# Kernel tuning notes

Hardware: AMD Instinct MI355X
Metric: run time of the kernel (lower is better)

## Reference

```python
import jax, jax.numpy as jnp
import numpy as np
from jax import lax

T = 256        # sentence length
V = 50000      # vocab
NT = 50        # POS tags
NL = 40        # dependency labels
WD, TD = 300, 100
IN = WD + TD   # 400, LSTM input & hidden size
H = IN
BI = 2 * H     # 800, biLSTM output per token
MI = 2 * BI    # 1600, MLP input/hidden size


def setup_inputs() -> dict:
    key = jax.random.key(0)
    ks = jax.random.split(key, 32)
    s = 0.05
    d = {
        'words': jax.random.randint(ks[0], (T,), 0, V),
        'tags': jax.random.randint(ks[1], (T,), 0, NT),
        'arcs': jax.random.randint(ks[2], (T + 1,), 0, T + 1),
        'h0': jax.random.normal(ks[3], (4, 1, H), jnp.float32),
        'c0': jax.random.normal(ks[4], (4, 1, H), jnp.float32),
        'word_emb': jax.random.normal(ks[5], (V, WD), jnp.float32) * s,
        'tag_emb': jax.random.normal(ks[6], (NT, TD), jnp.float32) * s,
        # LSTM layer 0: input IN; layer 1: input BI. Leading dim 2 = directions (fwd, rev).
        'Wih0': jax.random.normal(ks[7], (2, 4 * H, IN), jnp.float32) * s,
        'Whh0': jax.random.normal(ks[8], (2, 4 * H, H), jnp.float32) * s,
        'bih0': jax.random.normal(ks[9], (2, 4 * H), jnp.float32) * s,
        'bhh0': jax.random.normal(ks[10], (2, 4 * H), jnp.float32) * s,
        'Wih1': jax.random.normal(ks[11], (2, 4 * H, BI), jnp.float32) * s,
        'Whh1': jax.random.normal(ks[12], (2, 4 * H, H), jnp.float32) * s,
        'bih1': jax.random.normal(ks[13], (2, 4 * H), jnp.float32) * s,
        'bhh1': jax.random.normal(ks[14], (2, 4 * H), jnp.float32) * s,
        # arc-score MLP: 1600 -> 1600 -> 1 (Linear, Tanh, Linear)
        'Wa1': jax.random.normal(ks[15], (MI, MI), jnp.float32) * s,
        'ba1': jax.random.normal(ks[16], (MI,), jnp.float32) * s,
        'Wa2': jax.random.normal(ks[17], (1, MI), jnp.float32) * s,
        'ba2': jax.random.normal(ks[18], (1,), jnp.float32) * s,
        # label MLP: 1600 -> 1600 -> 40
        'Wl1': jax.random.normal(ks[19], (MI, MI), jnp.float32) * s,
        'bl1': jax.random.normal(ks[20], (MI,), jnp.float32) * s,
        'Wl2': jax.random.normal(ks[21], (NL, MI), jnp.float32) * s,
        'bl2': jax.random.normal(ks[22], (NL,), jnp.float32) * s,
    }
    return d


def _lstm_dir(x, Wih, Whh, bih, bhh, h, c):
    # x: [T, in]; returns [T, H]. Torch gate order i, f, g, o.
    xg = x @ Wih.T + (bih + bhh)  # precompute input projection: [T, 4H]

    def step(carry, xt):
        h, c = carry
        g = xt + h @ Whh.T
        i, f, gg, o = jnp.split(g, 4, axis=-1)
        i, f, o = jax.nn.sigmoid(i), jax.nn.sigmoid(f), jax.nn.sigmoid(o)
        c = f * c + i * jnp.tanh(gg)
        h = o * jnp.tanh(c)
        return (h, c), h

    (_, _), ys = lax.scan(step, (h, c), xg)
    return ys


def _bilstm_layer(x, Wih, Whh, bih, bhh, h0f, c0f, h0b, c0b):
    fwd = _lstm_dir(x, Wih[0], Whh[0], bih[0], bhh[0], h0f, c0f)
    bwd = _lstm_dir(x[::-1], Wih[1], Whh[1], bih[1], bhh[1], h0b, c0b)[::-1]
    return jnp.concatenate([fwd, bwd], axis=-1)


def _mlp(z, W1, b1, W2, b2):
    return jnp.tanh(z @ W1.T + b1) @ W2.T + b2


def reference(words, tags, arcs, h0, c0, word_emb, tag_emb,
              Wih0, Whh0, bih0, bhh0, Wih1, Whh1, bih1, bhh1,
              Wa1, ba1, Wa2, ba2, Wl1, bl1, Wl2, bl2):
    n = words.shape[0]
    x = jnp.concatenate([word_emb[words], tag_emb[tags]], axis=-1)  # [T, 400]
    x1 = _bilstm_layer(x, Wih0, Whh0, bih0, bhh0, h0[0, 0], c0[0, 0], h0[1, 0], c0[1, 0])
    hV = _bilstm_layer(x1, Wih1, Whh1, bih1, bhh1, h0[2, 0], c0[2, 0], h0[3, 0], c0[3, 0])  # [T, 800]

    # All-pairs arc scores: feats[h, d] = concat(hV[h], hV[d]) -> MLP -> scalar.
    hh = jnp.broadcast_to(hV[:, None, :], (n, n, BI))
    dd = jnp.broadcast_to(hV[None, :, :], (n, n, BI))
    feats = jnp.concatenate([hh, dd], axis=-1)  # [T, T, 1600]
    raw = _mlp(feats, Wa1, ba1, Wa2, ba2)[..., 0]  # [T, T]
    raw = raw * (1.0 - jnp.eye(n, dtype=raw.dtype))  # head == dep left at 0
    scores = jnp.zeros((n + 1, n + 1), raw.dtype).at[1:, 1:].set(raw).at[0, 0].set(1.0)

    # Labels: for token i with gold head h (1-based), concat(hV[i], hV[h-1]); head==0 -> zeros.
    heads = arcs[1:]
    idx = jnp.clip(heads - 1, 0, n - 1)
    lf = jnp.concatenate([hV, hV[idx]], axis=-1)  # [T, 1600]
    lab = _mlp(lf, Wl1, bl1, Wl2, bl2)  # [T, 40]
    lab = jnp.where((heads == 0)[:, None], jnp.zeros_like(lab), lab)
    return (scores, lab)
```

## Files before the change

### kernel.cpp

```cpp
#include <hip/hip_runtime.h>

typedef unsigned int   u32;
typedef unsigned long long u64;

__device__ __forceinline__ float fast_tanh(float x) {
    x = fminf(fmaxf(x, -15.f), 15.f);
    float e = __expf(2.f * x);
    return __fdividef(e - 1.f, e + 1.f);
}

#define OF_X    ((size_t)0)
#define OF_XG   (OF_X  + 409600)
#define OF_H    (OF_XG + 3276800)
#define OF_P    (OF_H  + 1638400)
#define OF_Q    (OF_P  + 1638400)
#define OF_U    (OF_Q  + 1638400)

__device__ __forceinline__ float4 hist4(const u64* __restrict__ hist, int t, int k) {
    const u64* p = (k < 400) ? hist + (size_t)t * 400 + k
                             : hist + 102400 + (size_t)(255 - t) * 400 + (k - 400);
    ulonglong2 a = *(const ulonglong2*)p;
    ulonglong2 b = *(const ulonglong2*)(p + 2);
    return make_float4(__uint_as_float((u32)a.x), __uint_as_float((u32)a.y),
                       __uint_as_float((u32)b.x), __uint_as_float((u32)b.y));
}

__global__ void embed_kernel(const int* __restrict__ words, const int* __restrict__ tags,
                             const float* __restrict__ wemb, const float* __restrict__ temb,
                             float* __restrict__ x) {
    int t = blockIdx.x;
    int w = words[t], tg = tags[t];
    for (int i = threadIdx.x; i < 400; i += 256) {
        float v = (i < 300) ? wemb[(size_t)w * 300 + i]
                            : temb[(size_t)tg * 100 + (i - 300)];
        x[(size_t)t * 400 + i] = v;
    }
}

__global__ __launch_bounds__(256)
void gemm_kernel(const float* __restrict__ A, int lda,
                 const float* __restrict__ B, int ldb, int boff,
                 const float* __restrict__ bias1, const float* __restrict__ bias2,
                 float* __restrict__ C, int ldc, int K, int act) {
    int t0 = blockIdx.x * 64;
    int n0 = blockIdx.y * 64;
    int tid = threadIdx.x;
    int tx = tid & 15, ty = tid >> 4;
    int lr = tid >> 2, lk = (tid & 3) * 4;
    __shared__ float As[16][68];
    __shared__ float Bs[16][68];
    float acc[4][4] = {};

    for (int k0 = 0; k0 < K; k0 += 16) {
        float4 av = *(const float4*)(A + (size_t)(t0 + lr) * lda + k0 + lk);
        float4 bv = *(const float4*)(B + (size_t)(n0 + lr) * ldb + boff + k0 + lk);
        __syncthreads();
        As[lk + 0][lr] = av.x; As[lk + 1][lr] = av.y; As[lk + 2][lr] = av.z; As[lk + 3][lr] = av.w;
        Bs[lk + 0][lr] = bv.x; Bs[lk + 1][lr] = bv.y; Bs[lk + 2][lr] = bv.z; Bs[lk + 3][lr] = bv.w;
        __syncthreads();
        #pragma unroll
        for (int kk = 0; kk < 16; ++kk) {
            float4 a4 = *(const float4*)&As[kk][ty * 4];
            float4 b4 = *(const float4*)&Bs[kk][tx * 4];
            acc[0][0] += a4.x * b4.x; acc[0][1] += a4.x * b4.y; acc[0][2] += a4.x * b4.z; acc[0][3] += a4.x * b4.w;
            acc[1][0] += a4.y * b4.x; acc[1][1] += a4.y * b4.y; acc[1][2] += a4.y * b4.z; acc[1][3] += a4.y * b4.w;
            acc[2][0] += a4.z * b4.x; acc[2][1] += a4.z * b4.y; acc[2][2] += a4.z * b4.z; acc[2][3] += a4.z * b4.w;
            acc[3][0] += a4.w * b4.x; acc[3][1] += a4.w * b4.y; acc[3][2] += a4.w * b4.z; acc[3][3] += a4.w * b4.w;
        }
    }
    float bs[4];
    #pragma unroll
    for (int j = 0; j < 4; ++j) {
        int n = n0 + tx * 4 + j;
        float b = 0.f;
        if (bias1) b += bias1[n];
        if (bias2) b += bias2[n];
        bs[j] = b;
    }
    #pragma unroll
    for (int i = 0; i < 4; ++i) {
        int t = t0 + ty * 4 + i;
        float4 o;
        o.x = acc[i][0] + bs[0]; o.y = acc[i][1] + bs[1];
        o.z = acc[i][2] + bs[2]; o.w = acc[i][3] + bs[3];
        if (act) { o.x = fast_tanh(o.x); o.y = fast_tanh(o.y); o.z = fast_tanh(o.z); o.w = fast_tanh(o.w); }
        *(float4*)(C + (size_t)t * ldc + n0 + tx * 4) = o;
    }
}

__global__ __launch_bounds__(256)
void gemm_hist_kernel(const u64* __restrict__ hist, const int* __restrict__ arcs,
                      const float* __restrict__ B, int ldb, int boff,
                      const float* __restrict__ bias1, const float* __restrict__ bias2,
                      float* __restrict__ C, int ldc, int K, int act) {
    int t0 = blockIdx.x * 64;
    int n0 = blockIdx.y * 64;
    int tid = threadIdx.x;
    int tx = tid & 15, ty = tid >> 4;
    int lr = tid >> 2, lk = (tid & 3) * 4;
    __shared__ float As[16][68];
    __shared__ float Bs[16][68];
    float acc[4][4] = {};

    int t = t0 + lr;
    int tind = t;
    if (arcs) {
        int h = arcs[1 + t];
        tind = min(max(h - 1, 0), 255);
    }

    for (int k0 = 0; k0 < K; k0 += 16) {
        int k = k0 + lk;
        int tt = (k < 800) ? t : tind;
        int kk2 = (k < 800) ? k : k - 800;
        float4 av = hist4(hist, tt, kk2);
        float4 bv = *(const float4*)(B + (size_t)(n0 + lr) * ldb + boff + k0 + lk);
        __syncthreads();
        As[lk + 0][lr] = av.x; As[lk + 1][lr] = av.y; As[lk + 2][lr] = av.z; As[lk + 3][lr] = av.w;
        Bs[lk + 0][lr] = bv.x; Bs[lk + 1][lr] = bv.y; Bs[lk + 2][lr] = bv.z; Bs[lk + 3][lr] = bv.w;
        __syncthreads();
        #pragma unroll
        for (int kk = 0; kk < 16; ++kk) {
            float4 a4 = *(const float4*)&As[kk][ty * 4];
            float4 b4 = *(const float4*)&Bs[kk][tx * 4];
            acc[0][0] += a4.x * b4.x; acc[0][1] += a4.x * b4.y; acc[0][2] += a4.x * b4.z; acc[0][3] += a4.x * b4.w;
            acc[1][0] += a4.y * b4.x; acc[1][1] += a4.y * b4.y; acc[1][2] += a4.y * b4.z; acc[1][3] += a4.y * b4.w;
            acc[2][0] += a4.z * b4.x; acc[2][1] += a4.z * b4.y; acc[2][2] += a4.z * b4.z; acc[2][3] += a4.z * b4.w;
            acc[3][0] += a4.w * b4.x; acc[3][1] += a4.w * b4.y; acc[3][2] += a4.w * b4.z; acc[3][3] += a4.w * b4.w;
        }
    }
    float bs[4];
    #pragma unroll
    for (int j = 0; j < 4; ++j) {
        int n = n0 + tx * 4 + j;
        float b = 0.f;
        if (bias1) b += bias1[n];
        if (bias2) b += bias2[n];
        bs[j] = b;
    }
    #pragma unroll
    for (int i = 0; i < 4; ++i) {
        int tr = t0 + ty * 4 + i;
        float4 o;
        o.x = acc[i][0] + bs[0]; o.y = acc[i][1] + bs[1];
        o.z = acc[i][2] + bs[2]; o.w = acc[i][3] + bs[3];
        if (act) { o.x = fast_tanh(o.x); o.y = fast_tanh(o.y); o.z = fast_tanh(o.z); o.w = fast_tanh(o.w); }
        *(float4*)(C + (size_t)tr * ldc + n0 + tx * 4) = o;
    }
}

#define LSTM_G 50
__global__ __launch_bounds__(256)
void lstm_kernel(const float* __restrict__ Whh,
                 const float* __restrict__ h0,
                 const float* __restrict__ c0,
                 int hc_base,
                 const float* __restrict__ xg,
                 u64* __restrict__ hist,
                 u32 tag_base) {
    const int T = 256;
    int bid = blockIdx.x;
    int d  = bid / LSTM_G;
    int wg = bid % LSTM_G;
    int a8 = wg * 8;
    int tid = threadIdx.x;
    int w = tid >> 6, lane = tid & 63;
    int c = lane & 7, r = lane >> 3;
    int gate = r >> 1, jj = r & 1;
    int gr = gate * 400 + a8 + 2 * w + jj;

    __shared__ float hbuf[2][416];

    float4 wv[13];
    const float* wrow = Whh + (size_t)d * 640000 + (size_t)gr * 400;
    #pragma unroll
    for (int i = 0; i < 13; ++i) {
        int k = 4 * (c + 8 * i);
        if (k + 3 < 400) {
            wv[i] = *(const float4*)(wrow + k);
        } else {
            wv[i] = make_float4(0.f, 0.f, 0.f, 0.f);
        }
    }
    if (tid < 16) { hbuf[0][400 + tid] = 0.f; hbuf[1][400 + tid] = 0.f; }

    float c_state = 0.f;
    if (lane == 0 || lane == 8)
        c_state = c0[(hc_base + d) * 400 + a8 + 2 * w + jj];

    u64* hst = hist + (size_t)d * 102400;
    bool need2 = (tid + 256 < 400);

    for (int t = 0; t < T; ++t) {
        int xt = d ? (T - 1 - t) : t;
        float xgv = xg[(size_t)xt * 3200 + d * 1600 + gr];
        float* hb = hbuf[t & 1];

        if (t == 0) {
            hb[tid] = h0[(hc_base + d) * 400 + tid];
            if (need2) hb[tid + 256] = h0[(hc_base + d) * 400 + tid + 256];
        } else {
            const u64* src = hst + (size_t)(t - 1) * 400;
            u32 want = tag_base + (u32)t;
            bool d1 = false, d2 = !need2;
            while (!(d1 && d2)) {
                u64 v1 = 0, v2 = 0;
                if (!d1) v1 = __hip_atomic_load(&src[tid], __ATOMIC_RELAXED, __HIP_MEMORY_SCOPE_AGENT);
                if (!d2) v2 = __hip_atomic_load(&src[tid + 256], __ATOMIC_RELAXED, __HIP_MEMORY_SCOPE_AGENT);
                if (!d1 && (u32)(v1 >> 32) == want) { hb[tid] = __uint_as_float((u32)v1); d1 = true; }
                if (!d2 && (u32)(v2 >> 32) == want) { hb[tid + 256] = __uint_as_float((u32)v2); d2 = true; }
            }
        }
        __syncthreads();

        const float4* h4 = (const float4*)hb;
        float s = 0.f;
        #pragma unroll
        for (int i = 0; i < 13; ++i) {
            float4 hv = h4[c + 8 * i];
            s += wv[i].x * hv.x + wv[i].y * hv.y + wv[i].z * hv.z + wv[i].w * hv.w;
        }
        s += __shfl_down(s, 4);
        s += __shfl_down(s, 2);
        s += __shfl_down(s, 1);

        float v = 0.f;
        if (c == 0) {
            float tot = s + xgv;
            float arg = (gate == 2) ? 2.f * tot : -tot;
            arg = fminf(fmaxf(arg, -60.f), 60.f);
            float e = __expf(arg);
            v = (gate == 2) ? (e - 1.f) * __frcp_rn(e + 1.f)
                            : __frcp_rn(1.f + e);
        }
        float fv = __shfl(v, lane + 16);
        float gv = __shfl(v, lane + 32);
        float ov = __shfl(v, lane + 48);
        if (lane == 0 || lane == 8) {
            c_state = fv * c_state + v * gv;
            float ec = __expf(fminf(fmaxf(2.f * c_state, -60.f), 60.f));
            float th = (ec - 1.f) * __frcp_rn(ec + 1.f);
            float h = ov * th;
            u64 pk = (((u64)(tag_base + t + 1)) << 32) | (u64)__float_as_uint(h);
            __hip_atomic_store(&hst[(size_t)t * 400 + a8 + 2 * w + jj], pk,
                               __ATOMIC_RELAXED, __HIP_MEMORY_SCOPE_AGENT);
        }
    }
}

__global__ __launch_bounds__(256)
void arc_kernel(const float* __restrict__ P, const float* __restrict__ Q,
                const float* __restrict__ Wa2, const float* __restrict__ ba2,
                float* __restrict__ out) {
    int i0 = blockIdx.x * 16, j0 = blockIdx.y * 16;
    int tid = threadIdx.x;
    int ii = tid >> 4, jj = tid & 15;
    __shared__ float Pt[16][65], Qt[16][65];
    __shared__ float W2f[1600];
    for (int m = tid; m < 1600; m += 256) W2f[m] = Wa2[m];
    __syncthreads();

    float acc = 0.f;
    int mm = tid & 63, r4 = tid >> 6;
    for (int m0 = 0; m0 < 1600; m0 += 64) {
        #pragma unroll
        for (int rr = r4; rr < 16; rr += 4) {
            Pt[rr][mm] = P[(size_t)(i0 + rr) * 1600 + m0 + mm];
            Qt[rr][mm] = Q[(size_t)(j0 + rr) * 1600 + m0 + mm];
        }
        __syncthreads();
        #pragma unroll 8
        for (int m = 0; m < 64; ++m) {
            float s = Pt[ii][m] + Qt[jj][m];
            acc += W2f[m0 + m] * fast_tanh(s);
        }
        __syncthreads();
    }
    float raw = acc + ba2[0];
    int gi = i0 + ii, gj = j0 + jj;
    if (gi == gj) raw = 0.f;
    out[(size_t)(gi + 1) * 257 + (gj + 1)] = raw;
}

__global__ void border_kernel(float* __restrict__ out) {
    int t = threadIdx.x;
    if (t < 257) out[t] = (t == 0) ? 1.0f : 0.0f;
    if (t >= 1 && t < 257) out[(size_t)t * 257] = 0.0f;
}

__global__ __launch_bounds__(256)
void label_out_kernel(const float* __restrict__ U, const float* __restrict__ Wl2,
                      const float* __restrict__ bl2, const int* __restrict__ arcs,
                      float* __restrict__ out) {
    int t = blockIdx.x;
    __shared__ float u_l[1600];
    __shared__ float part[4][64];
    for (int m = threadIdx.x; m < 1600; m += 256) u_l[m] = U[(size_t)t * 1600 + m];
    __syncthreads();
    int tid = threadIdx.x;
    int n = tid & 63, p = tid >> 6;
    float acc = 0.f;
    if (n < 40) {
        const float4* wr4 = (const float4*)(Wl2 + (size_t)n * 1600 + p * 400);
        const float*  ub  = u_l + p * 400;
        for (int m = 0; m < 100; ++m) {
            float4 w = wr4[m];
            acc += ub[4*m] * w.x + ub[4*m+1] * w.y + ub[4*m+2] * w.z + ub[4*m+3] * w.w;
        }
    }
    part[p][n] = acc;
    __syncthreads();
    if (tid < 40) {
        float v = part[0][tid] + part[1][tid] + part[2][tid] + part[3][tid] + bl2[tid];
        if (arcs[1 + t] == 0) v = 0.f;
        out[(size_t)t * 40 + tid] = v;
    }
}

extern "C" void kernel_launch(void* const* d_in, const int* in_sizes, int n_in,
                              void* d_out, int out_size, void* d_ws, size_t ws_size,
                              hipStream_t stream) {
    const int*   words = (const int*)d_in[0];
    const int*   tags  = (const int*)d_in[1];
    const int*   arcs  = (const int*)d_in[2];
    const float* h0    = (const float*)d_in[3];
    const float* c0    = (const float*)d_in[4];
    const float* wemb  = (const float*)d_in[5];
    const float* temb  = (const float*)d_in[6];
    const float* Wih0  = (const float*)d_in[7];
    const float* Whh0  = (const float*)d_in[8];
    const float* bih0  = (const float*)d_in[9];
    const float* bhh0  = (const float*)d_in[10];
    const float* Wih1  = (const float*)d_in[11];
    const float* Whh1  = (const float*)d_in[12];
    const float* bih1  = (const float*)d_in[13];
    const float* bhh1  = (const float*)d_in[14];
    const float* Wa1   = (const float*)d_in[15];
    const float* ba1   = (const float*)d_in[16];
    const float* Wa2   = (const float*)d_in[17];
    const float* ba2   = (const float*)d_in[18];
    const float* Wl1   = (const float*)d_in[19];
    const float* bl1   = (const float*)d_in[20];
    const float* Wl2   = (const float*)d_in[21];
    const float* bl2   = (const float*)d_in[22];
    float* out = (float*)d_out;

    char* ws = (char*)d_ws;
    float* x    = (float*)(ws + OF_X);
    float* xg   = (float*)(ws + OF_XG);
    u64*   hist = (u64*)  (ws + OF_H);
    float* P    = (float*)(ws + OF_P);
    float* Q    = (float*)(ws + OF_Q);
    float* U    = (float*)(ws + OF_U);

    embed_kernel<<<256, 256, 0, stream>>>(words, tags, wemb, temb, x);
    gemm_kernel<<<dim3(4, 50), 256, 0, stream>>>(x, 400, Wih0, 400, 0, bih0, bhh0, xg, 3200, 400, 0);
    lstm_kernel<<<2 * LSTM_G, 256, 0, stream>>>(Whh0, h0, c0, 0, xg, hist, 0u);
    gemm_hist_kernel<<<dim3(4, 50), 256, 0, stream>>>(hist, nullptr, Wih1, 800, 0, bih1, bhh1, xg, 3200, 800, 0);
    lstm_kernel<<<2 * LSTM_G, 256, 0, stream>>>(Whh1, h0, c0, 2, xg, hist, 256u);
    gemm_hist_kernel<<<dim3(4, 25), 256, 0, stream>>>(hist, nullptr, Wa1, 1600, 0,   ba1,    nullptr, P, 1600, 800, 0);
    gemm_hist_kernel<<<dim3(4, 25), 256, 0, stream>>>(hist, nullptr, Wa1, 1600, 800, nullptr, nullptr, Q, 1600, 800, 0);
    arc_kernel<<<dim3(16, 16), 256, 0, stream>>>(P, Q, Wa2, ba2, out);
    border_kernel<<<1, 320, 0, stream>>>(out);
    gemm_hist_kernel<<<dim3(4, 25), 256, 0, stream>>>(hist, arcs, Wl1, 1600, 0, bl1, nullptr, U, 1600, 1600, 1);
    label_out_kernel<<<256, 256, 0, stream>>>(U, Wl2, bl2, arcs, out + 66049);
}
```

Baseline: 1.343 ms.

## Fuse embedding into input GEMM, merge P/Q GEMMs, fold border into arc kernel

Embedding lookup now happens inside the first input-projection GEMM, so the intermediate x buffer and its kernel go away. The two arc-MLP half GEMMs become one launch writing an interleaved PQ buffer, and the arc kernel now writes the score-matrix border itself. This removes three kernel launches and one round trip of intermediate data. It adds gather-indexed loads inside the GEMM.

```diff
diff --git a/kernel.cpp b/kernel.cpp
--- a/kernel.cpp
+++ b/kernel.cpp
@@ -9,12 +9,10 @@
     return __fdividef(e - 1.f, e + 1.f);
 }
 
-#define OF_X    ((size_t)0)
-#define OF_XG   (OF_X  + 409600)
+#define OF_XG   ((size_t)0)
 #define OF_H    (OF_XG + 3276800)
-#define OF_P    (OF_H  + 1638400)
-#define OF_Q    (OF_P  + 1638400)
-#define OF_U    (OF_Q  + 1638400)
+#define OF_PQ   (OF_H  + 1638400)
+#define OF_U    (OF_PQ + 3276800)
 
 __device__ __forceinline__ float4 hist4(const u64* __restrict__ hist, int t, int k) {
     const u64* p = (k < 400) ? hist + (size_t)t * 400 + k
@@ -25,23 +23,12 @@
                        __uint_as_float((u32)b.x), __uint_as_float((u32)b.y));
 }
 
-__global__ void embed_kernel(const int* __restrict__ words, const int* __restrict__ tags,
-                             const float* __restrict__ wemb, const float* __restrict__ temb,
-                             float* __restrict__ x) {
-    int t = blockIdx.x;
-    int w = words[t], tg = tags[t];
-    for (int i = threadIdx.x; i < 400; i += 256) {
-        float v = (i < 300) ? wemb[(size_t)w * 300 + i]
-                            : temb[(size_t)tg * 100 + (i - 300)];
-        x[(size_t)t * 400 + i] = v;
-    }
-}
-
-__global__ __launch_bounds__(256)
-void gemm_kernel(const float* __restrict__ A, int lda,
-                 const float* __restrict__ B, int ldb, int boff,
-                 const float* __restrict__ bias1, const float* __restrict__ bias2,
-                 float* __restrict__ C, int ldc, int K, int act) {
+__global__ __launch_bounds__(256)
+void gemm_embed_kernel(const int* __restrict__ words, const int* __restrict__ tags,
+                       const float* __restrict__ wemb, const float* __restrict__ temb,
+                       const float* __restrict__ B,
+                       const float* __restrict__ bias1, const float* __restrict__ bias2,
+                       float* __restrict__ C) {
     int t0 = blockIdx.x * 64;
     int n0 = blockIdx.y * 64;
     int tid = threadIdx.x;
@@ -51,9 +38,14 @@
     __shared__ float Bs[16][68];
     float acc[4][4] = {};
 
-    for (int k0 = 0; k0 < K; k0 += 16) {
-        float4 av = *(const float4*)(A + (size_t)(t0 + lr) * lda + k0 + lk);
-        float4 bv = *(const float4*)(B + (size_t)(n0 + lr) * ldb + boff + k0 + lk);
+    int t = t0 + lr;
+    const float* arow0 = wemb + (size_t)words[t] * 300;
+    const float* arow1 = temb + (size_t)tags[t] * 100 - 300;
+
+    for (int k0 = 0; k0 < 400; k0 += 16) {
+        int k = k0 + lk;
+        float4 av = (k < 300) ? *(const float4*)(arow0 + k) : *(const float4*)(arow1 + k);
+        float4 bv = *(const float4*)(B + (size_t)(n0 + lr) * 400 + k);
         __syncthreads();
         As[lk + 0][lr] = av.x; As[lk + 1][lr] = av.y; As[lk + 2][lr] = av.z; As[lk + 3][lr] = av.w;
         Bs[lk + 0][lr] = bv.x; Bs[lk + 1][lr] = bv.y; Bs[lk + 2][lr] = bv.z; Bs[lk + 3][lr] = bv.w;
@@ -72,19 +64,15 @@
     #pragma unroll
     for (int j = 0; j < 4; ++j) {
         int n = n0 + tx * 4 + j;
-        float b = 0.f;
-        if (bias1) b += bias1[n];
-        if (bias2) b += bias2[n];
-        bs[j] = b;
+        bs[j] = bias1[n] + bias2[n];
     }
     #pragma unroll
     for (int i = 0; i < 4; ++i) {
-        int t = t0 + ty * 4 + i;
+        int tr = t0 + ty * 4 + i;
         float4 o;
         o.x = acc[i][0] + bs[0]; o.y = acc[i][1] + bs[1];
         o.z = acc[i][2] + bs[2]; o.w = acc[i][3] + bs[3];
-        if (act) { o.x = fast_tanh(o.x); o.y = fast_tanh(o.y); o.z = fast_tanh(o.z); o.w = fast_tanh(o.w); }
-        *(float4*)(C + (size_t)t * ldc + n0 + tx * 4) = o;
+        *(float4*)(C + (size_t)tr * 3200 + n0 + tx * 4) = o;
     }
 }
 
@@ -146,6 +134,56 @@
         o.z = acc[i][2] + bs[2]; o.w = acc[i][3] + bs[3];
         if (act) { o.x = fast_tanh(o.x); o.y = fast_tanh(o.y); o.z = fast_tanh(o.z); o.w = fast_tanh(o.w); }
         *(float4*)(C + (size_t)tr * ldc + n0 + tx * 4) = o;
+    }
+}
+
+__global__ __launch_bounds__(256)
+void gemm_pq_kernel(const u64* __restrict__ hist, const float* __restrict__ Wa1,
+                    const float* __restrict__ ba1, float* __restrict__ PQ) {
+    int t0 = blockIdx.x * 64;
+    int n0 = blockIdx.y * 64;
+    int tid = threadIdx.x;
+    int tx = tid & 15, ty = tid >> 4;
+    int lr = tid >> 2, lk = (tid & 3) * 4;
+    __shared__ float As[16][68];
+    __shared__ float Bs[16][68];
+    float acc[4][4] = {};
+
+    int t = t0 + lr;
+    int nn = n0 + lr;
+    const float* brow = (nn < 1600) ? Wa1 + (size_t)nn * 1600
+                                    : Wa1 + (size_t)(nn - 1600) * 1600 + 800;
+
+    for (int k0 = 0; k0 < 800; k0 += 16) {
+        float4 av = hist4(hist, t, k0 + lk);
+        float4 bv = *(const float4*)(brow + k0 + lk);
+        __syncthreads();
+        As[lk + 0][lr] = av.x; As[lk + 1][lr] = av.y; As[lk + 2][lr] = av.z; As[lk + 3][lr] = av.w;
+        Bs[lk + 0][lr] = bv.x; Bs[lk + 1][lr] = bv.y; Bs[lk + 2][lr] = bv.z; Bs[lk + 3][lr] = bv.w;
+        __syncthreads();
+        #pragma unroll
+        for (int kk = 0; kk < 16; ++kk) {
+            float4 a4 = *(const float4*)&As[kk][ty * 4];
+            float4 b4 = *(const float4*)&Bs[kk][tx * 4];
+            acc[0][0] += a4.x * b4.x; acc[0][1] += a4.x * b4.y; acc[0][2] += a4.x * b4.z; acc[0][3] += a4.x * b4.w;
+            acc[1][0] += a4.y * b4.x; acc[1][1] += a4.y * b4.y; acc[1][2] += a4.y * b4.z; acc[1][3] += a4.y * b4.w;
+            acc[2][0] += a4.z * b4.x; acc[2][1] += a4.z * b4.y; acc[2][2] += a4.z * b4.z; acc[2][3] += a4.z * b4.w;
+            acc[3][0] += a4.w * b4.x; acc[3][1] += a4.w * b4.y; acc[3][2] += a4.w * b4.z; acc[3][3] += a4.w * b4.w;
+        }
+    }
+    float bs[4];
+    #pragma unroll
+    for (int j = 0; j < 4; ++j) {
+        int n = n0 + tx * 4 + j;
+        bs[j] = (n < 1600) ? ba1[n] : 0.f;
+    }
+    #pragma unroll
+    for (int i = 0; i < 4; ++i) {
+        int tr = t0 + ty * 4 + i;
+        float4 o;
+        o.x = acc[i][0] + bs[0]; o.y = acc[i][1] + bs[1];
+        o.z = acc[i][2] + bs[2]; o.w = acc[i][3] + bs[3];
+        *(float4*)(PQ + (size_t)tr * 3200 + n0 + tx * 4) = o;
     }
 }
 
@@ -176,11 +214,7 @@
     #pragma unroll
     for (int i = 0; i < 13; ++i) {
         int k = 4 * (c + 8 * i);
-        if (k + 3 < 400) {
-            wv[i] = *(const float4*)(wrow + k);
-        } else {
-            wv[i] = make_float4(0.f, 0.f, 0.f, 0.f);
-        }
+        wv[i] = (k + 3 < 400) ? *(const float4*)(wrow + k) : make_float4(0.f, 0.f, 0.f, 0.f);
     }
     if (tid < 16) { hbuf[0][400 + tid] = 0.f; hbuf[1][400 + tid] = 0.f; }
 
@@ -249,7 +283,7 @@
 }
 
 __global__ __launch_bounds__(256)
-void arc_kernel(const float* __restrict__ P, const float* __restrict__ Q,
+void arc_kernel(const float* __restrict__ PQ,
                 const float* __restrict__ Wa2, const float* __restrict__ ba2,
                 float* __restrict__ out) {
     int i0 = blockIdx.x * 16, j0 = blockIdx.y * 16;
@@ -257,6 +291,12 @@
     int ii = tid >> 4, jj = tid & 15;
     __shared__ float Pt[16][65], Qt[16][65];
     __shared__ float W2f[1600];
+
+    if (i0 == 0 && j0 == 0) {
+        if (tid < 257) out[tid] = (tid == 0) ? 1.0f : 0.0f;
+        out[(size_t)(tid + 1) * 257] = 0.0f;
+        if (tid == 0) out[0] = 1.0f;
+    }
     for (int m = tid; m < 1600; m += 256) W2f[m] = Wa2[m];
     __syncthreads();
 
@@ -265,8 +305,8 @@
     for (int m0 = 0; m0 < 1600; m0 += 64) {
         #pragma unroll
         for (int rr = r4; rr < 16; rr += 4) {
-            Pt[rr][mm] = P[(size_t)(i0 + rr) * 1600 + m0 + mm];
-            Qt[rr][mm] = Q[(size_t)(j0 + rr) * 1600 + m0 + mm];
+            Pt[rr][mm] = PQ[(size_t)(i0 + rr) * 3200 + m0 + mm];
+            Qt[rr][mm] = PQ[(size_t)(j0 + rr) * 3200 + 1600 + m0 + mm];
         }
         __syncthreads();
         #pragma unroll 8
@@ -280,12 +320,6 @@
     int gi = i0 + ii, gj = j0 + jj;
     if (gi == gj) raw = 0.f;
     out[(size_t)(gi + 1) * 257 + (gj + 1)] = raw;
-}
-
-__global__ void border_kernel(float* __restrict__ out) {
-    int t = threadIdx.x;
-    if (t < 257) out[t] = (t == 0) ? 1.0f : 0.0f;
-    if (t >= 1 && t < 257) out[(size_t)t * 257] = 0.0f;
 }
 
 __global__ __launch_bounds__(256)
@@ -346,22 +380,17 @@
     float* out = (float*)d_out;
 
     char* ws = (char*)d_ws;
-    float* x    = (float*)(ws + OF_X);
     float* xg   = (float*)(ws + OF_XG);
     u64*   hist = (u64*)  (ws + OF_H);
-    float* P    = (float*)(ws + OF_P);
-    float* Q    = (float*)(ws + OF_Q);
+    float* PQ   = (float*)(ws + OF_PQ);
     float* U    = (float*)(ws + OF_U);
 
-    embed_kernel<<<256, 256, 0, stream>>>(words, tags, wemb, temb, x);
-    gemm_kernel<<<dim3(4, 50), 256, 0, stream>>>(x, 400, Wih0, 400, 0, bih0, bhh0, xg, 3200, 400, 0);
+    gemm_embed_kernel<<<dim3(4, 50), 256, 0, stream>>>(words, tags, wemb, temb, Wih0, bih0, bhh0, xg);
     lstm_kernel<<<2 * LSTM_G, 256, 0, stream>>>(Whh0, h0, c0, 0, xg, hist, 0u);
     gemm_hist_kernel<<<dim3(4, 50), 256, 0, stream>>>(hist, nullptr, Wih1, 800, 0, bih1, bhh1, xg, 3200, 800, 0);
     lstm_kernel<<<2 * LSTM_G, 256, 0, stream>>>(Whh1, h0, c0, 2, xg, hist, 256u);
-    gemm_hist_kernel<<<dim3(4, 25), 256, 0, stream>>>(hist, nullptr, Wa1, 1600, 0,   ba1,    nullptr, P, 1600, 800, 0);
-    gemm_hist_kernel<<<dim3(4, 25), 256, 0, stream>>>(hist, nullptr, Wa1, 1600, 800, nullptr, nullptr, Q, 1600, 800, 0);
-    arc_kernel<<<dim3(16, 16), 256, 0, stream>>>(P, Q, Wa2, ba2, out);
-    border_kernel<<<1, 320, 0, stream>>>(out);
+    gemm_pq_kernel<<<dim3(4, 50), 256, 0, stream>>>(hist, Wa1, ba1, PQ);
+    arc_kernel<<<dim3(16, 16), 256, 0, stream>>>(PQ, Wa2, ba2, out);
     gemm_hist_kernel<<<dim3(4, 25), 256, 0, stream>>>(hist, arcs, Wl1, 1600, 0, bl1, nullptr, U, 1600, 1600, 1);
     label_out_kernel<<<256, 256, 0, stream>>>(U, Wl2, bl2, arcs, out + 66049);
 }
```

Result: faster. 1.273 ms (-5.2%).
